# Kernel optimization log

Hardware: AMD Instinct MI355X
Metric: run time of the kernel (lower is better)

Reference implementation:

```python
import jax, jax.numpy as jnp
import numpy as np

MEM_DIM = 2000
FEA_DIM = 256
SHRINK_THRES = 0.0025
EPS = 1e-06


def setup_inputs() -> dict:
    key = jax.random.key(0)
    k1, k2 = jax.random.split(key)
    x = jax.random.normal(k1, (65536, FEA_DIM), dtype=jnp.float32)
    stdv = 1.0 / np.sqrt(FEA_DIM)
    weight = jax.random.uniform(k2, (MEM_DIM, FEA_DIM), dtype=jnp.float32,
                                minval=-stdv, maxval=stdv)
    temperature = jnp.asarray(0.5, dtype=jnp.float32)
    return {"input": x, "weight": weight, "temperature": temperature}


def hard_shrink_relu(a, lambd=SHRINK_THRES, epsilon=EPS):
    a = jnp.clip(a, -10.0, 10.0)
    denom = jnp.maximum(jnp.abs(a - lambd) + epsilon, epsilon)
    out = jax.nn.relu(a - lambd) * a / denom
    return jnp.where(jnp.isnan(out) | jnp.isinf(out), 0.0, out)


def reference(input, weight, temperature):
    mem_dim = weight.shape[0]
    inv_m = 1.0 / mem_dim
    x = jnp.clip(input, -10.0, 10.0)                      # [N, F]
    att = jnp.einsum('nf,mf->nm', x, weight)              # [N, M]
    att = jax.nn.softmax(att / temperature, axis=1)
    # shrink_thres > 0 branch
    att = hard_shrink_relu(att)
    weight_sum = jnp.sum(att, axis=1, keepdims=True)      # [N, 1]
    zero_mask = weight_sum < 1e-08
    att = att / (weight_sum + 1e-08)
    att = jnp.where(zero_mask, inv_m, att)                # rows with ~zero sum -> uniform
    att = jnp.where(jnp.isnan(att) | jnp.isinf(att), inv_m, att)
    output = jnp.einsum('nm,mf->nf', att, weight)         # [N, F]
    return output, att
```

## Files before the change

### kernel.cpp

```cpp
#include <hip/hip_runtime.h>
#include <hip/hip_bf16.h>
#include <cstdint>

#define N_ROWS 65536
#define FEA    256
#define MEM    2000
#define MEMP   2048
#define LAMBD  0.0025f
#define SEPS   1e-6f
#define NW     16

typedef __attribute__((ext_vector_type(8))) _Float16 f16x8;
typedef __attribute__((ext_vector_type(8))) short    bf16x8;
typedef __attribute__((ext_vector_type(4))) float    f32x4;

__device__ __forceinline__ short f2bf(float f) {
    union { float f; uint32_t u; } v; v.f = f;
    uint32_t r = v.u + 0x7fffu + ((v.u >> 16) & 1u);
    return (short)(r >> 16);
}

__global__ __launch_bounds__(256) void prep_kernel(const float* __restrict__ W,
                                                   const float* __restrict__ temp,
                                                   _Float16* __restrict__ Whl2,
                                                   short* __restrict__ Wt) {
    __shared__ float tile[8][260];
    const int t  = threadIdx.x;
    const int m0 = blockIdx.x * 8;
    const int row = t >> 5, col = (t & 31) * 8;
    const int m = m0 + row;
    const float invT = 1.0f / temp[0];
    if (m < MEM) {
        f32x4 a = *(const f32x4*)(W + (size_t)m * FEA + col);
        f32x4 b = *(const f32x4*)(W + (size_t)m * FEA + col + 4);
        #pragma unroll
        for (int u = 0; u < 4; ++u) { tile[row][col+u] = a[u]; tile[row][col+4+u] = b[u]; }
    } else {
        #pragma unroll
        for (int u = 0; u < 8; ++u) tile[row][col+u] = 0.f;
    }
    __syncthreads();
    {
        const int c = col >> 5, q = (col >> 3) & 3;
        const int tt = m >> 4, lr = m & 15;
        _Float16 hi[8], lo[8];
        #pragma unroll
        for (int j = 0; j < 8; ++j) {
            float w = tile[row][col + j] * invT;
            _Float16 h = (_Float16)w;
            hi[j] = h;
            lo[j] = (_Float16)((w - (float)h) * 2048.0f);
        }
        _Float16* dst = Whl2 + (((size_t)(tt * 8 + c)) << 10) + (q * 16 + lr) * 16;
        *(f16x8*)dst       = *(f16x8*)&hi[0];
        *(f16x8*)(dst + 8) = *(f16x8*)&lo[0];
    }
    {
        short buf[8];
        #pragma unroll
        for (int j = 0; j < 8; ++j) buf[j] = f2bf(tile[j][t]);
        *(bf16x8*)(Wt + (size_t)t * MEMP + m0) = *(bf16x8*)&buf[0];
    }
}

__global__ __launch_bounds__(1024, 4) void score_kernel(const float* __restrict__ x,
                                                        const _Float16* __restrict__ Whl2,
                                                        float* __restrict__ att) {
    __shared__ __align__(16) _Float16 ah_s[32][264];
    __shared__ __align__(16) _Float16 al_s[32][264];
    __shared__ float redbuf[NW][32];
    __shared__ float redglob[32];

    const int tid  = threadIdx.x;
    const int lane = tid & 63;
    const int wid  = tid >> 6;
    const int lr   = lane & 15;
    const int q    = lane >> 4;
    const size_t r0 = (size_t)blockIdx.x * 32;

    {
        const int srow = tid >> 5, scol = (tid & 31) * 8;
        const float* xp = x + (r0 + srow) * FEA + scol;
        f32x4 v0 = *(const f32x4*)xp;
        f32x4 v1 = *(const f32x4*)(xp + 4);
        #pragma unroll
        for (int w = 0; w < 4; ++w) {
            float f0 = fminf(fmaxf(v0[w], -10.f), 10.f);
            float f1 = fminf(fmaxf(v1[w], -10.f), 10.f);
            _Float16 h0 = (_Float16)f0, h1 = (_Float16)f1;
            ah_s[srow][scol + w]     = h0;
            ah_s[srow][scol + 4 + w] = h1;
            al_s[srow][scol + w]     = (_Float16)((f0 - (float)h0) * 2048.0f);
            al_s[srow][scol + 4 + w] = (_Float16)((f1 - (float)h1) * 2048.0f);
        }
    }
    __syncthreads();

    f32x4 acc[2][8];
    #pragma unroll
    for (int rg = 0; rg < 2; ++rg)
        #pragma unroll
        for (int jj = 0; jj < 8; ++jj) acc[rg][jj] = (f32x4){0.f, 0.f, 0.f, 0.f};

    const f32x4 z0 = (f32x4){0.f, 0.f, 0.f, 0.f};

    #pragma unroll 1
    for (int c = 0; c < 8; ++c) {
        f16x8 ah[2], al[2];
        #pragma unroll
        for (int rg = 0; rg < 2; ++rg) {
            ah[rg] = *(const f16x8*)&ah_s[rg * 16 + lr][c * 32 + q * 8];
            al[rg] = *(const f16x8*)&al_s[rg * 16 + lr][c * 32 + q * 8];
        }
        #pragma unroll
        for (int jj = 0; jj < 8; ++jj) {
            const int t = wid + 16 * jj;
            const _Float16* bp = Whl2 + (((size_t)(t * 8 + c)) << 10) + lane * 16;
            f16x8 bh = *(const f16x8*)bp;
            f16x8 bl = *(const f16x8*)(bp + 8);
            #pragma unroll
            for (int rg = 0; rg < 2; ++rg) {
                f32x4 t1 = __builtin_amdgcn_mfma_f32_16x16x32_f16(al[rg], bh, z0, 0, 0, 0);
                t1 = __builtin_amdgcn_mfma_f32_16x16x32_f16(ah[rg], bl, t1, 0, 0, 0);
                acc[rg][jj] = __builtin_amdgcn_mfma_f32_16x16x32_f16(ah[rg], bh, acc[rg][jj], 0, 0, 0);
                acc[rg][jj] += t1 * (1.0f / 2048.0f);
            }
        }
    }

    const bool lastv = (wid < 13);

    auto xred = [&](float v[2][4], bool ismax) {
        #pragma unroll
        for (int m = 1; m < 16; m <<= 1)
            #pragma unroll
            for (int rg = 0; rg < 2; ++rg)
                #pragma unroll
                for (int i = 0; i < 4; ++i) {
                    float o = __shfl_xor(v[rg][i], m, 64);
                    v[rg][i] = ismax ? fmaxf(v[rg][i], o) : (v[rg][i] + o);
                }
        if (lr == 0) {
            #pragma unroll
            for (int rg = 0; rg < 2; ++rg)
                #pragma unroll
                for (int i = 0; i < 4; ++i) redbuf[wid][rg * 16 + q * 4 + i] = v[rg][i];
        }
        __syncthreads();
        if (tid < 32) {
            float r = redbuf[0][tid];
            #pragma unroll
            for (int w = 1; w < NW; ++w) {
                float o = redbuf[w][tid];
                r = ismax ? fmaxf(r, o) : (r + o);
            }
            redglob[tid] = r;
        }
        __syncthreads();
        #pragma unroll
        for (int rg = 0; rg < 2; ++rg)
            #pragma unroll
            for (int i = 0; i < 4; ++i) v[rg][i] = redglob[rg * 16 + q * 4 + i];
        __syncthreads();
    };

    float M[2][4];
    #pragma unroll
    for (int rg = 0; rg < 2; ++rg)
        #pragma unroll
        for (int i = 0; i < 4; ++i) M[rg][i] = -3.0e38f;
    #pragma unroll
    for (int jj = 0; jj < 8; ++jj) {
        if (jj < 7 || lastv) {
            #pragma unroll
            for (int rg = 0; rg < 2; ++rg)
                #pragma unroll
                for (int i = 0; i < 4; ++i) M[rg][i] = fmaxf(M[rg][i], acc[rg][jj][i]);
        }
    }
    xred(M, true);

    #pragma unroll
    for (int jj = 0; jj < 8; ++jj) {
        const bool v = (jj < 7) || lastv;
        #pragma unroll
        for (int rg = 0; rg < 2; ++rg)
            #pragma unroll
            for (int i = 0; i < 4; ++i)
                acc[rg][jj][i] = v ? __expf(acc[rg][jj][i] - M[rg][i]) : 0.0f;
    }

    float Z[2][4];
    #pragma unroll
    for (int rg = 0; rg < 2; ++rg)
        #pragma unroll
        for (int i = 0; i < 4; ++i) Z[rg][i] = 0.f;
    #pragma unroll
    for (int jj = 0; jj < 8; ++jj)
        #pragma unroll
        for (int rg = 0; rg < 2; ++rg)
            #pragma unroll
            for (int i = 0; i < 4; ++i) Z[rg][i] += acc[rg][jj][i];
    xred(Z, false);

    #pragma unroll
    for (int rg = 0; rg < 2; ++rg)
        #pragma unroll
        for (int i = 0; i < 4; ++i) Z[rg][i] = __builtin_amdgcn_rcpf(Z[rg][i]);
    #pragma unroll
    for (int jj = 0; jj < 8; ++jj)
        #pragma unroll
        for (int rg = 0; rg < 2; ++rg)
            #pragma unroll
            for (int i = 0; i < 4; ++i) {
                float a = acc[rg][jj][i] * Z[rg][i];
                float d = a - LAMBD;
                float o = d * a * __builtin_amdgcn_rcpf(d + SEPS);
                acc[rg][jj][i] = (d > 0.f) ? o : 0.f;
            }

    float WS[2][4];
    #pragma unroll
    for (int rg = 0; rg < 2; ++rg)
        #pragma unroll
        for (int i = 0; i < 4; ++i) WS[rg][i] = 0.f;
    #pragma unroll
    for (int jj = 0; jj < 8; ++jj)
        #pragma unroll
        for (int rg = 0; rg < 2; ++rg)
            #pragma unroll
            for (int i = 0; i < 4; ++i) WS[rg][i] += acc[rg][jj][i];
    xred(WS, false);

    const float inv_m = 1.0f / (float)MEM;
    float scl[2][4];
    bool  zr[2][4];
    #pragma unroll
    for (int rg = 0; rg < 2; ++rg)
        #pragma unroll
        for (int i = 0; i < 4; ++i) {
            scl[rg][i] = __builtin_amdgcn_rcpf(WS[rg][i] + 1e-8f);
            zr[rg][i]  = (WS[rg][i] < 1e-8f);
        }

    #pragma unroll
    for (int rg = 0; rg < 2; ++rg)
        #pragma unroll
        for (int i = 0; i < 4; ++i) {
            float* p = att + (r0 + rg * 16 + q * 4 + i) * (size_t)MEM + wid * 16 + lr;
            #pragma unroll
            for (int jj = 0; jj < 8; ++jj) {
                if (jj < 7 || lastv) {
                    float vv = zr[rg][i] ? inv_m : acc[rg][jj][i] * scl[rg][i];
                    p[jj * 256] = vv;
                }
            }
        }
}

__global__ __launch_bounds__(512) void gemm2_kernel(const float* __restrict__ att,
                                                    const short* __restrict__ Wt,
                                                    float* __restrict__ out) {
    __shared__ short Asm[2][128][40];
    __shared__ short Bsm[2][256][40];
    const int tid  = threadIdx.x;
    const int lane = tid & 63;
    const int wid  = tid >> 6;
    const int rg   = wid >> 2;
    const int cg   = wid & 3;
    const int lr   = lane & 15;
    const int lk   = (lane >> 4) * 8;
    const size_t r0 = (size_t)blockIdx.x * 128;

    const int sa_row = tid >> 2, sa_ko = (tid & 3) * 8;
    const int sb_f   = tid >> 1, sb_ko = (tid & 1) * 16;

    auto stage = [&](int buf, int kc) {
        const int k0 = kc * 32;
        {
            int k = k0 + sa_ko;
            short b[8];
            if (k < MEM) {
                const float* ap = att + (r0 + sa_row) * (size_t)MEM + k;
                f32x4 v0 = *(const f32x4*)ap;
                f32x4 v1 = *(const f32x4*)(ap + 4);
                #pragma unroll
                for (int u = 0; u < 4; ++u) { b[u] = f2bf(v0[u]); b[4+u] = f2bf(v1[u]); }
            } else {
                #pragma unroll
                for (int u = 0; u < 8; ++u) b[u] = 0;
            }
            *(bf16x8*)&Asm[buf][sa_row][sa_ko] = *(bf16x8*)&b[0];
        }
        {
            const short* wp = Wt + (size_t)sb_f * MEMP + k0 + sb_ko;
            bf16x8 b0 = *(const bf16x8*)wp;
            bf16x8 b1 = *(const bf16x8*)(wp + 8);
            *(bf16x8*)&Bsm[buf][sb_f][sb_ko]     = b0;
            *(bf16x8*)&Bsm[buf][sb_f][sb_ko + 8] = b1;
        }
    };

    f32x4 acc[4][4];
    #pragma unroll
    for (int i = 0; i < 4; ++i)
        #pragma unroll
        for (int j = 0; j < 4; ++j) acc[i][j] = (f32x4){0.f, 0.f, 0.f, 0.f};

    stage(0, 0);
    int cur = 0;
    for (int kc = 0; kc < 63; ++kc) {
        __syncthreads();
        if (kc + 1 < 63) stage(cur ^ 1, kc + 1);
        bf16x8 a_[4], b_[4];
        #pragma unroll
        for (int i = 0; i < 4; ++i) a_[i] = *(const bf16x8*)&Asm[cur][rg * 64 + i * 16 + lr][lk];
        #pragma unroll
        for (int j = 0; j < 4; ++j) b_[j] = *(const bf16x8*)&Bsm[cur][cg * 64 + j * 16 + lr][lk];
        #pragma unroll
        for (int i = 0; i < 4; ++i)
            #pragma unroll
            for (int j = 0; j < 4; ++j)
                acc[i][j] = __builtin_amdgcn_mfma_f32_16x16x32_bf16(a_[i], b_[j], acc[i][j], 0, 0, 0);
        cur ^= 1;
    }

    #pragma unroll
    for (int i = 0; i < 4; ++i)
        #pragma unroll
        for (int j = 0; j < 4; ++j)
            #pragma unroll
            for (int ii = 0; ii < 4; ++ii) {
                size_t row = r0 + rg * 64 + i * 16 + (lane >> 4) * 4 + ii;
                out[row * FEA + cg * 64 + j * 16 + lr] = acc[i][j][ii];
            }
}

extern "C" void kernel_launch(void* const* d_in, const int* in_sizes, int n_in,
                              void* d_out, int out_size, void* d_ws, size_t ws_size,
                              hipStream_t stream) {
    const float* x = (const float*)d_in[0];
    const float* W = (const float*)d_in[1];
    const float* T = (const float*)d_in[2];
    float* out = (float*)d_out;
    float* att = out + (size_t)N_ROWS * FEA;
    _Float16* Whl2 = (_Float16*)d_ws;
    short*    Wt   = (short*)((char*)d_ws + (2u << 20));

    prep_kernel<<<dim3(256), dim3(256), 0, stream>>>(W, T, Whl2, Wt);
    score_kernel<<<dim3(N_ROWS / 32), dim3(1024), 0, stream>>>(x, Whl2, att);
    gemm2_kernel<<<dim3(N_ROWS / 128), dim3(512), 0, stream>>>(att, Wt, out);
}
```

Measured before the change: 526.8 us.

## Shrink score kernel tile to 16 rows with 8 waves per block

The score kernel now handles 16 rows per block with 512 threads (8 waves), each wave covering 16 column tiles instead of 8 tiles for two row groups. The cross-wave reduction drops the second shared-memory broadcast stage, so every lane reads redbuf directly and one barrier is saved per reduction. This cuts per-block barrier cost and adds more, smaller blocks. In exchange, each block fetches the W fragments from global/L2 for only 16 rows, doubling B-operand traffic per row.

```diff
diff --git a/kernel.cpp b/kernel.cpp
--- a/kernel.cpp
+++ b/kernel.cpp
@@ -8,7 +8,6 @@
 #define MEMP   2048
 #define LAMBD  0.0025f
 #define SEPS   1e-6f
-#define NW     16
 
 typedef __attribute__((ext_vector_type(8))) _Float16 f16x8;
 typedef __attribute__((ext_vector_type(8))) short    bf16x8;
@@ -63,20 +62,19 @@
     }
 }
 
-__global__ __launch_bounds__(1024, 4) void score_kernel(const float* __restrict__ x,
-                                                        const _Float16* __restrict__ Whl2,
-                                                        float* __restrict__ att) {
-    __shared__ __align__(16) _Float16 ah_s[32][264];
-    __shared__ __align__(16) _Float16 al_s[32][264];
-    __shared__ float redbuf[NW][32];
-    __shared__ float redglob[32];
+__global__ __launch_bounds__(512, 4) void score_kernel(const float* __restrict__ x,
+                                                       const _Float16* __restrict__ Whl2,
+                                                       float* __restrict__ att) {
+    __shared__ __align__(16) _Float16 ah_s[16][264];
+    __shared__ __align__(16) _Float16 al_s[16][264];
+    __shared__ float redbuf[8][16];
 
     const int tid  = threadIdx.x;
     const int lane = tid & 63;
     const int wid  = tid >> 6;
     const int lr   = lane & 15;
     const int q    = lane >> 4;
-    const size_t r0 = (size_t)blockIdx.x * 32;
+    const size_t r0 = (size_t)blockIdx.x * 16;
 
     {
         const int srow = tid >> 5, scol = (tid & 31) * 8;
@@ -96,166 +94,127 @@
     }
     __syncthreads();
 
-    f32x4 acc[2][8];
-    #pragma unroll
-    for (int rg = 0; rg < 2; ++rg)
-        #pragma unroll
-        for (int jj = 0; jj < 8; ++jj) acc[rg][jj] = (f32x4){0.f, 0.f, 0.f, 0.f};
+    f32x4 acc[16];
+    #pragma unroll
+    for (int jj = 0; jj < 16; ++jj) acc[jj] = (f32x4){0.f, 0.f, 0.f, 0.f};
 
     const f32x4 z0 = (f32x4){0.f, 0.f, 0.f, 0.f};
 
     #pragma unroll 1
     for (int c = 0; c < 8; ++c) {
-        f16x8 ah[2], al[2];
-        #pragma unroll
-        for (int rg = 0; rg < 2; ++rg) {
-            ah[rg] = *(const f16x8*)&ah_s[rg * 16 + lr][c * 32 + q * 8];
-            al[rg] = *(const f16x8*)&al_s[rg * 16 + lr][c * 32 + q * 8];
-        }
-        #pragma unroll
-        for (int jj = 0; jj < 8; ++jj) {
-            const int t = wid + 16 * jj;
+        f16x8 ah = *(const f16x8*)&ah_s[lr][c * 32 + q * 8];
+        f16x8 al = *(const f16x8*)&al_s[lr][c * 32 + q * 8];
+        #pragma unroll 8
+        for (int jj = 0; jj < 16; ++jj) {
+            const int t = wid + 8 * jj;
             const _Float16* bp = Whl2 + (((size_t)(t * 8 + c)) << 10) + lane * 16;
             f16x8 bh = *(const f16x8*)bp;
             f16x8 bl = *(const f16x8*)(bp + 8);
-            #pragma unroll
-            for (int rg = 0; rg < 2; ++rg) {
-                f32x4 t1 = __builtin_amdgcn_mfma_f32_16x16x32_f16(al[rg], bh, z0, 0, 0, 0);
-                t1 = __builtin_amdgcn_mfma_f32_16x16x32_f16(ah[rg], bl, t1, 0, 0, 0);
-                acc[rg][jj] = __builtin_amdgcn_mfma_f32_16x16x32_f16(ah[rg], bh, acc[rg][jj], 0, 0, 0);
-                acc[rg][jj] += t1 * (1.0f / 2048.0f);
-            }
-        }
-    }
-
-    const bool lastv = (wid < 13);
-
-    auto xred = [&](float v[2][4], bool ismax) {
+            f32x4 t1 = __builtin_amdgcn_mfma_f32_16x16x32_f16(al, bh, z0, 0, 0, 0);
+            t1 = __builtin_amdgcn_mfma_f32_16x16x32_f16(ah, bl, t1, 0, 0, 0);
+            acc[jj] = __builtin_amdgcn_mfma_f32_16x16x32_f16(ah, bh, acc[jj], 0, 0, 0);
+            acc[jj] += t1 * (1.0f / 2048.0f);
+        }
+    }
+
+    const bool lastv = (wid < 5);
+
+    auto xred = [&](float v[4], bool ismax) {
         #pragma unroll
         for (int m = 1; m < 16; m <<= 1)
             #pragma unroll
-            for (int rg = 0; rg < 2; ++rg)
-                #pragma unroll
-                for (int i = 0; i < 4; ++i) {
-                    float o = __shfl_xor(v[rg][i], m, 64);
-                    v[rg][i] = ismax ? fmaxf(v[rg][i], o) : (v[rg][i] + o);
-                }
+            for (int i = 0; i < 4; ++i) {
+                float o = __shfl_xor(v[i], m, 64);
+                v[i] = ismax ? fmaxf(v[i], o) : (v[i] + o);
+            }
         if (lr == 0) {
             #pragma unroll
-            for (int rg = 0; rg < 2; ++rg)
-                #pragma unroll
-                for (int i = 0; i < 4; ++i) redbuf[wid][rg * 16 + q * 4 + i] = v[rg][i];
+            for (int i = 0; i < 4; ++i) redbuf[wid][q * 4 + i] = v[i];
         }
         __syncthreads();
-        if (tid < 32) {
-            float r = redbuf[0][tid];
-            #pragma unroll
-            for (int w = 1; w < NW; ++w) {
-                float o = redbuf[w][tid];
+        #pragma unroll
+        for (int i = 0; i < 4; ++i) {
+            float r = redbuf[0][q * 4 + i];
+            #pragma unroll
+            for (int w = 1; w < 8; ++w) {
+                float o = redbuf[w][q * 4 + i];
                 r = ismax ? fmaxf(r, o) : (r + o);
             }
-            redglob[tid] = r;
-        }
-        __syncthreads();
-        #pragma unroll
-        for (int rg = 0; rg < 2; ++rg)
-            #pragma unroll
-            for (int i = 0; i < 4; ++i) v[rg][i] = redglob[rg * 16 + q * 4 + i];
+            v[i] = r;
+        }
         __syncthreads();
     };
 
-    float M[2][4];
-    #pragma unroll
-    for (int rg = 0; rg < 2; ++rg)
-        #pragma unroll
-        for (int i = 0; i < 4; ++i) M[rg][i] = -3.0e38f;
-    #pragma unroll
-    for (int jj = 0; jj < 8; ++jj) {
-        if (jj < 7 || lastv) {
-            #pragma unroll
-            for (int rg = 0; rg < 2; ++rg)
-                #pragma unroll
-                for (int i = 0; i < 4; ++i) M[rg][i] = fmaxf(M[rg][i], acc[rg][jj][i]);
+    float M[4];
+    #pragma unroll
+    for (int i = 0; i < 4; ++i) M[i] = -3.0e38f;
+    #pragma unroll
+    for (int jj = 0; jj < 16; ++jj) {
+        if (jj < 15 || lastv) {
+            #pragma unroll
+            for (int i = 0; i < 4; ++i) M[i] = fmaxf(M[i], acc[jj][i]);
         }
     }
     xred(M, true);
 
     #pragma unroll
-    for (int jj = 0; jj < 8; ++jj) {
-        const bool v = (jj < 7) || lastv;
-        #pragma unroll
-        for (int rg = 0; rg < 2; ++rg)
-            #pragma unroll
-            for (int i = 0; i < 4; ++i)
-                acc[rg][jj][i] = v ? __expf(acc[rg][jj][i] - M[rg][i]) : 0.0f;
-    }
-
-    float Z[2][4];
-    #pragma unroll
-    for (int rg = 0; rg < 2; ++rg)
-        #pragma unroll
-        for (int i = 0; i < 4; ++i) Z[rg][i] = 0.f;
-    #pragma unroll
-    for (int jj = 0; jj < 8; ++jj)
-        #pragma unroll
-        for (int rg = 0; rg < 2; ++rg)
-            #pragma unroll
-            for (int i = 0; i < 4; ++i) Z[rg][i] += acc[rg][jj][i];
+    for (int jj = 0; jj < 16; ++jj) {
+        const bool v = (jj < 15) || lastv;
+        #pragma unroll
+        for (int i = 0; i < 4; ++i)
+            acc[jj][i] = v ? __expf(acc[jj][i] - M[i]) : 0.0f;
+    }
+
+    float Z[4];
+    #pragma unroll
+    for (int i = 0; i < 4; ++i) Z[i] = 0.f;
+    #pragma unroll
+    for (int jj = 0; jj < 16; ++jj)
+        #pragma unroll
+        for (int i = 0; i < 4; ++i) Z[i] += acc[jj][i];
     xred(Z, false);
 
     #pragma unroll
-    for (int rg = 0; rg < 2; ++rg)
-        #pragma unroll
-        for (int i = 0; i < 4; ++i) Z[rg][i] = __builtin_amdgcn_rcpf(Z[rg][i]);
-    #pragma unroll
-    for (int jj = 0; jj < 8; ++jj)
-        #pragma unroll
-        for (int rg = 0; rg < 2; ++rg)
-            #pragma unroll
-            for (int i = 0; i < 4; ++i) {
-                float a = acc[rg][jj][i] * Z[rg][i];
-                float d = a - LAMBD;
-                float o = d * a * __builtin_amdgcn_rcpf(d + SEPS);
-                acc[rg][jj][i] = (d > 0.f) ? o : 0.f;
-            }
-
-    float WS[2][4];
-    #pragma unroll
-    for (int rg = 0; rg < 2; ++rg)
-        #pragma unroll
-        for (int i = 0; i < 4; ++i) WS[rg][i] = 0.f;
-    #pragma unroll
-    for (int jj = 0; jj < 8; ++jj)
-        #pragma unroll
-        for (int rg = 0; rg < 2; ++rg)
-            #pragma unroll
-            for (int i = 0; i < 4; ++i) WS[rg][i] += acc[rg][jj][i];
+    for (int i = 0; i < 4; ++i) Z[i] = __builtin_amdgcn_rcpf(Z[i]);
+    #pragma unroll
+    for (int jj = 0; jj < 16; ++jj)
+        #pragma unroll
+        for (int i = 0; i < 4; ++i) {
+            float a = acc[jj][i] * Z[i];
+            float d = a - LAMBD;
+            float o = d * a * __builtin_amdgcn_rcpf(d + SEPS);
+            acc[jj][i] = (d > 0.f) ? o : 0.f;
+        }
+
+    float WS[4];
+    #pragma unroll
+    for (int i = 0; i < 4; ++i) WS[i] = 0.f;
+    #pragma unroll
+    for (int jj = 0; jj < 16; ++jj)
+        #pragma unroll
+        for (int i = 0; i < 4; ++i) WS[i] += acc[jj][i];
     xred(WS, false);
 
     const float inv_m = 1.0f / (float)MEM;
-    float scl[2][4];
-    bool  zr[2][4];
-    #pragma unroll
-    for (int rg = 0; rg < 2; ++rg)
-        #pragma unroll
-        for (int i = 0; i < 4; ++i) {
-            scl[rg][i] = __builtin_amdgcn_rcpf(WS[rg][i] + 1e-8f);
-            zr[rg][i]  = (WS[rg][i] < 1e-8f);
-        }
-
-    #pragma unroll
-    for (int rg = 0; rg < 2; ++rg)
-        #pragma unroll
-        for (int i = 0; i < 4; ++i) {
-            float* p = att + (r0 + rg * 16 + q * 4 + i) * (size_t)MEM + wid * 16 + lr;
-            #pragma unroll
-            for (int jj = 0; jj < 8; ++jj) {
-                if (jj < 7 || lastv) {
-                    float vv = zr[rg][i] ? inv_m : acc[rg][jj][i] * scl[rg][i];
-                    p[jj * 256] = vv;
-                }
-            }
-        }
+    float scl[4];
+    bool  zr[4];
+    #pragma unroll
+    for (int i = 0; i < 4; ++i) {
+        scl[i] = __builtin_amdgcn_rcpf(WS[i] + 1e-8f);
+        zr[i]  = (WS[i] < 1e-8f);
+    }
+
+    #pragma unroll
+    for (int i = 0; i < 4; ++i) {
+        float* p = att + (r0 + q * 4 + i) * (size_t)MEM + wid * 16 + lr;
+        #pragma unroll
+        for (int jj = 0; jj < 16; ++jj) {
+            if (jj < 15 || lastv) {
+                float vv = zr[i] ? inv_m : acc[jj][i] * scl[i];
+                p[jj * 128] = vv;
+            }
+        }
+    }
 }
 
 __global__ __launch_bounds__(512) void gemm2_kernel(const float* __restrict__ att,
@@ -348,6 +307,6 @@
     short*    Wt   = (short*)((char*)d_ws + (2u << 20));
 
     prep_kernel<<<dim3(256), dim3(256), 0, stream>>>(W, T, Whl2, Wt);
-    score_kernel<<<dim3(N_ROWS / 32), dim3(1024), 0, stream>>>(x, Whl2, att);
+    score_kernel<<<dim3(N_ROWS / 16), dim3(512), 0, stream>>>(x, Whl2, att);
     gemm2_kernel<<<dim3(N_ROWS / 128), dim3(512), 0, stream>>>(att, Wt, out);
 }
```

New measurement: 2.058 ms. 3.91x slower.
